# Kernel optimization log

Hardware: AMD Instinct MI355X
Metric: run time of the kernel (lower is better)

The kernel has to match this reference:

```python
import jax, jax.numpy as jnp
import numpy as np

B, ROWS, COLS, D, H = 64, 7, 7, 1280, 256
S, NEG, GRU_ROWS = 5, 16, 6  # pred_steps, neg_samples, rows processed by GRU


def setup_inputs() -> dict:
    key = jax.random.key(0)
    ks = jax.random.split(key, 10)
    sc = 0.05  # keep gates/tanh out of saturation
    return {
        "encodings": jax.random.normal(ks[0], (B, ROWS, COLS, D), jnp.float32),
        "hidden": jnp.zeros((1, 1, H), jnp.float32),
        "gru_w_ih": jax.random.normal(ks[1], (3 * H, D), jnp.float32) * sc,
        "gru_w_hh": jax.random.normal(ks[2], (3 * H, H), jnp.float32) * sc,
        "gru_b_ih": jax.random.normal(ks[3], (3 * H,), jnp.float32) * sc,
        "gru_b_hh": jax.random.normal(ks[4], (3 * H,), jnp.float32) * sc,
        "wk_w": jax.random.normal(ks[5], (S, D, H), jnp.float32) * sc,
        "wk_b": jax.random.normal(ks[6], (S, D), jnp.float32) * sc,
        "neg_rows": jax.random.randint(ks[7], (B, S, GRU_ROWS, COLS, NEG), 0, ROWS, jnp.int32),
        "neg_cols": jax.random.randint(ks[8], (B, S, GRU_ROWS, COLS, NEG), 0, COLS, jnp.int32),
    }


def _gru_contexts(encodings, hidden, w_ih, w_hh, b_ih, b_hh):
    # One GRU run per (image, column) over the first 6 rows, all batched together.
    x_seq = jnp.transpose(encodings[:, :GRU_ROWS], (1, 0, 2, 3)).reshape(GRU_ROWS, B * COLS, D)
    h0 = jnp.broadcast_to(hidden.reshape(1, H), (B * COLS, H))

    def step(h, x):
        gi = x @ w_ih.T + b_ih          # [N, 3H]
        gh = h @ w_hh.T + b_hh
        i_r, i_z, i_n = jnp.split(gi, 3, axis=-1)
        h_r, h_z, h_n = jnp.split(gh, 3, axis=-1)
        r = jax.nn.sigmoid(i_r + h_r)
        z = jax.nn.sigmoid(i_z + h_z)
        n = jnp.tanh(i_n + r * h_n)
        h_new = (1.0 - z) * n + z * h
        return h_new, h_new

    _, cs = jax.lax.scan(step, h0, x_seq)              # [6, B*7, H]
    return jnp.transpose(cs.reshape(GRU_ROWS, B, COLS, H), (1, 0, 2, 3))  # [B,6,7,H]


def reference(encodings, hidden, gru_w_ih, gru_w_hh, gru_b_ih, gru_b_hh,
              wk_w, wk_b, neg_rows, neg_cols):
    contexts = _gru_contexts(encodings, hidden, gru_w_ih, gru_w_hh, gru_b_ih, gru_b_hh)

    # Predictions for every step/row/col: hardtanh(Wk[s] c + b)   [B,S,6,7,D]
    preds = jnp.clip(jnp.einsum("brch,sdh->bsrcd", contexts, wk_w)
                     + wk_b[None, :, None, None, :], -1.0, 1.0)

    # Dot of every prediction with every patch encoding of the same image.
    enc_flat = encodings.reshape(B, ROWS * COLS, D)
    dots_all = jnp.einsum("bsrcd,bqd->bsrcq", preds, enc_flat)  # [B,S,6,7,49]

    # Positive: target is encodings[img, row, col] (as in the source).
    qpos = (jnp.arange(GRU_ROWS)[:, None] * COLS + jnp.arange(COLS)[None, :])  # [6,7]
    pos = jnp.take_along_axis(dots_all, qpos[None, None, :, :, None], axis=-1)  # [B,S,6,7,1]

    # Negatives: random (row,col) patches of the same image.
    neg_q = neg_rows * COLS + neg_cols                            # [B,S,6,7,NEG]
    neg = jnp.take_along_axis(dots_all, neg_q, axis=-1)

    dots = jnp.concatenate([pos, neg], axis=-1)                   # [B,S,6,7,1+NEG]
    loss_each = -jax.nn.log_softmax(dots, axis=-1)[..., 0]
    correct = (jnp.argmax(dots, axis=-1) == 0).astype(jnp.float32)

    # Valid predictions: row in range(6 - step)
    mask = ((jnp.arange(S)[:, None] + jnp.arange(GRU_ROWS)[None, :]) < GRU_ROWS)
    mask = mask.astype(jnp.float32)[None, :, :, None]             # [1,S,6,1]
    num_preds = jnp.sum(mask) * B * COLS

    loss = jnp.sum(loss_each * mask) / num_preds
    acc = jnp.sum(correct * mask) / num_preds
    return loss, acc
```

## Files before the change

kernel.cpp:

```cpp
#include <hip/hip_runtime.h>
#include <math.h>


typedef __bf16 bf16x8 __attribute__((ext_vector_type(8)));
typedef float  f32x4  __attribute__((ext_vector_type(4)));
typedef unsigned short u16;
typedef unsigned int u32;

__device__ inline u16 f2bf(float f) {
  unsigned int u = __float_as_uint(f);
  u += 0x7fff + ((u >> 16) & 1);
  return (u16)(u >> 16);
}

__device__ inline float bf2f(u16 b) {
  u32 u = (u32)b << 16;
  return __builtin_bit_cast(float, u);
}

__device__ inline void f2bf8(const float* s, u16* o) {
  float4 v0 = *(const float4*)s, v1 = *(const float4*)(s + 4);
  o[0] = f2bf(v0.x); o[1] = f2bf(v0.y); o[2] = f2bf(v0.z); o[3] = f2bf(v0.w);
  o[4] = f2bf(v1.x); o[5] = f2bf(v1.y); o[6] = f2bf(v1.z); o[7] = f2bf(v1.w);
}

__device__ inline bf16x8 lds_frag(const char* sm, int off) {
  return __builtin_bit_cast(bf16x8, *(const uint4*)(sm + off));
}

__device__ inline void gld_lds16(const void* g, void* l) {
  __builtin_amdgcn_global_load_lds(
      (const __attribute__((address_space(1))) u32*)g,
      (__attribute__((address_space(3))) u32*)l, 16, 0, 0);
}

__device__ inline float fast_sigmoid(float x) {
  float t = __builtin_amdgcn_exp2f(-1.44269504f * x);
  return __builtin_amdgcn_rcpf(1.f + t);
}
__device__ inline float fast_tanh(float x) {
  float xc = fminf(fmaxf(x, -9.f), 9.f);
  float t = __builtin_amdgcn_exp2f(2.88539008f * xc);
  return (t - 1.f) * __builtin_amdgcn_rcpf(t + 1.f);
}
__device__ inline float fast_exp(float x) {
  return __builtin_amdgcn_exp2f(1.44269504f * x);
}
__device__ inline float fast_log(float x) {
  return __builtin_amdgcn_logf(x) * 0.69314718f;
}

#define MFMA16(a, b, c) __builtin_amdgcn_mfma_f32_16x16x32_bf16(a, b, c, 0, 0, 0)

__global__ __launch_bounds__(256) void pack_all(
    const float* __restrict__ w_hh, const float* __restrict__ wk_w,
    const float* __restrict__ enc,  const float* __restrict__ w_ih,
    u16* __restrict__ whhpk, u16* __restrict__ wkwpk, u16* __restrict__ epk,
    u16* __restrict__ enc2,  u16* __restrict__ wih2, float* __restrict__ out)
{
  int tid = blockIdx.x * 256 + threadIdx.x;
  int lane = tid & 63;
  if (tid == 0) { out[0] = 0.f; out[1] = 0.f; }
  u16 o[8];
  if (tid < 655360) {
    int f = tid >> 6;
    int ks2 = f & 1, t1 = f >> 1;
    int w = t1 & 3, t2 = t1 >> 2;
    int ch = t2 % 20, b = t2 / 20;
    int q = w * 16 + (lane & 15);
    int d = ch * 64 + ks2 * 32 + (lane >> 4) * 8;
    if (q < 49) {
      f2bf8(&enc[(size_t)(b * 49 + q) * 1280 + d], o);
    } else {
#pragma unroll
      for (int j = 0; j < 8; ++j) o[j] = 0;
    }
    *(uint4*)&epk[(size_t)f * 512 + lane * 8] = *(uint4*)o;
    if (q < 42) {
      int r = q / 7, c = q - r * 7;
      int m = r * 448 + b * 7 + c;
      int by = m >> 7, row = m & 127;
      int k0 = d >> 6, slot = (d & 63) >> 3;
      int sl = slot ^ (row & 7);
      *(uint4*)&enc2[(size_t)((by * 20 + k0) * 1024 + row * 8 + sl) * 8] = *(uint4*)o;
    }
  } else if (tid < 679936) {
    int u = tid - 655360;
    int rest = u >> 6;
    int cb = rest >> 3, ks = rest & 7;
    int w = cb / 6, nf = cb % 6;
    int g = nf >> 1, half = nf & 1;
    int col = g * 256 + w * 32 + half * 16 + (lane & 15);
    int k = ks * 32 + (lane >> 4) * 8;
    f2bf8(&w_hh[(size_t)col * 256 + k], o);
    *(uint4*)&whhpk[(size_t)u * 8] = *(uint4*)o;
  } else if (tid < 884736) {
    int u = tid - 679936;
    int f = u >> 6;
    int ks = f & 7, t1 = f >> 3;
    int w = t1 & 3, t2 = t1 >> 2;
    int ch = t2 % 20, s = t2 / 20;
    f2bf8(&wk_w[((size_t)s * 1280 + ch * 64 + w * 16 + (lane & 15)) * 256
                + ks * 32 + (lane >> 4) * 8], o);
    *(uint4*)&wkwpk[(size_t)f * 512 + lane * 8] = *(uint4*)o;
  } else if (tid < 1007616) {
    int u = tid - 884736;
    int unit = u & 1023;
    int row = unit >> 3, sl = unit & 7;
    int tk = u >> 10;
    int k0 = tk % 20, bx = tk / 20;
    int slot = sl ^ (row & 7);
    f2bf8(&w_ih[(size_t)(bx * 128 + row) * 1280 + k0 * 64 + slot * 8], o);
    *(uint4*)&wih2[(size_t)u * 8] = *(uint4*)o;
  }
}

__global__ __launch_bounds__(256) void gi_mfma(
    const u16* __restrict__ enc2, const u16* __restrict__ wih2,
    const float* __restrict__ b_ih, u16* __restrict__ gib)
{
  const int bx = blockIdx.x, by = blockIdx.y;
  const int t = threadIdx.x, lane = t & 63, w = t >> 6;
  const int wr = w >> 1, wc = w & 1;

  __shared__ char sm[65536];
  const int wu = t & ~63;

  f32x4 acc[4][4];
#pragma unroll
  for (int i = 0; i < 4; ++i)
#pragma unroll
    for (int j = 0; j < 4; ++j) acc[i][j] = (f32x4){0.f, 0.f, 0.f, 0.f};

  const char* ga0 = (const char*)enc2 + ((size_t)(by * 20) << 14);
  const char* gb0 = (const char*)wih2 + ((size_t)(bx * 20) << 14);

#pragma unroll
  for (int j = 0; j < 4; ++j) {
    gld_lds16(ga0 + (j * 256 + t) * 16, sm + (j * 256 + wu) * 16);
    gld_lds16(gb0 + (j * 256 + t) * 16, sm + 16384 + (j * 256 + wu) * 16);
  }

  for (int k0c = 0; k0c < 20; ++k0c) {
    char* cur = sm + (k0c & 1) * 32768;
    if (k0c + 1 < 20) {
      char* nxt = sm + ((k0c + 1) & 1) * 32768;
      const char* ga = ga0 + ((size_t)(k0c + 1) << 14);
      const char* gb = gb0 + ((size_t)(k0c + 1) << 14);
#pragma unroll
      for (int j = 0; j < 4; ++j) {
        gld_lds16(ga + (j * 256 + t) * 16, nxt + (j * 256 + wu) * 16);
        gld_lds16(gb + (j * 256 + t) * 16, nxt + 16384 + (j * 256 + wu) * 16);
      }
      asm volatile("s_waitcnt vmcnt(8)" ::: "memory");
    } else {
      asm volatile("s_waitcnt vmcnt(0)" ::: "memory");
    }
    __builtin_amdgcn_s_barrier();

#pragma unroll
    for (int ks = 0; ks < 2; ++ks) {
      bf16x8 a[4], b[4];
#pragma unroll
      for (int i = 0; i < 4; ++i) {
        int arow = wr * 64 + i * 16 + (lane & 15);
        int akb  = (ks * 64 + (lane >> 4) * 16) ^ ((arow & 7) << 4);
        a[i] = lds_frag(cur, arow * 128 + akb);
        int brow = wc * 64 + i * 16 + (lane & 15);
        int bkb  = (ks * 64 + (lane >> 4) * 16) ^ ((brow & 7) << 4);
        b[i] = lds_frag(cur + 16384, brow * 128 + bkb);
      }
#pragma unroll
      for (int i = 0; i < 4; ++i)
#pragma unroll
        for (int jn = 0; jn < 4; ++jn)
          acc[i][jn] = MFMA16(a[i], b[jn], acc[i][jn]);
    }
    __builtin_amdgcn_s_barrier();
  }

#pragma unroll
  for (int i = 0; i < 4; ++i)
#pragma unroll
    for (int jn = 0; jn < 4; ++jn) {
      int gcol = bx * 128 + wc * 64 + jn * 16 + (lane & 15);
      float bias = b_ih[gcol];
#pragma unroll
      for (int r4 = 0; r4 < 4; ++r4) {
        int grow = by * 128 + wr * 64 + i * 16 + (lane >> 4) * 4 + r4;
        gib[(size_t)grow * 768 + gcol] = f2bf(acc[i][jn][r4] + bias);
      }
    }
}

__global__ __launch_bounds__(512) void gru_fused(
    const u16* __restrict__ whh_pk, const float* __restrict__ b_hh,
    const float* __restrict__ hidden, const u16* __restrict__ gib,
    u16* __restrict__ ctxb)
{
  const int n0 = blockIdx.x * 16;
  const int t = threadIdx.x, lane = t & 63, w = t >> 6;

  __shared__ char sm[16384 + 2 * 24576];
  const int GI0 = 16384;

  const int l15 = lane & 15;
  const int seq0 = (lane >> 4) * 4;
  const int hc0 = w * 32 + l15, hc1 = w * 32 + 16 + l15;

  const float br0 = b_hh[hc0],       br1 = b_hh[hc1];
  const float bz0 = b_hh[256 + hc0], bz1 = b_hh[256 + hc1];
  const float bn0 = b_hh[512 + hc0], bn1 = b_hh[512 + hc1];

#pragma unroll
  for (int i = 0; i < 3; ++i) {
    int chunk = w * 3 + i;
    gld_lds16(gib + (size_t)n0 * 768 + chunk * 512 + lane * 8,
              sm + GI0 + chunk * 1024);
  }

  float hold[2][4];
  {
    float h0 = hidden[hc0], h1 = hidden[hc1];
#pragma unroll
    for (int r4 = 0; r4 < 4; ++r4) { hold[0][r4] = h0; hold[1][r4] = h1; }
    u16 hb0 = f2bf(h0), hb1 = f2bf(h1);
#pragma unroll
    for (int r4 = 0; r4 < 4; ++r4) {
      int seq = seq0 + r4;
      *(u16*)(sm + seq * 512 + ((hc0 * 2) ^ ((seq & 7) << 4))) = hb0;
      *(u16*)(sm + seq * 512 + ((hc1 * 2) ^ ((seq & 7) << 4))) = hb1;
    }
  }

  bf16x8 bP[3][6];
  {
    const char* pkb0 = (const char*)whh_pk + w * 49152 + lane * 16;
#pragma unroll
    for (int j = 0; j < 3; ++j)
#pragma unroll
      for (int nf = 0; nf < 6; ++nf)
        bP[j][nf] = *(const bf16x8*)(pkb0 + nf * 8192 + j * 1024);
  }
  __syncthreads();

  for (int r = 0; r < 6; ++r) {
    const char* hb  = sm + (r & 1) * 8192;
    char* hbn       = sm + ((r + 1) & 1) * 8192;
    const char* gbr = sm + GI0 + (r & 1) * 24576;

    uintptr_t pa = (uintptr_t)whh_pk;
    asm volatile("" : "+v"(pa));
    const char* pkb = (const char*)pa + w * 49152 + lane * 16;

    f32x4 acc[6];
#pragma unroll
    for (int nf = 0; nf < 6; ++nf) acc[nf] = (f32x4){0.f, 0.f, 0.f, 0.f};

#pragma unroll
    for (int ks = 0; ks < 8; ++ks) {
      const int slot = ks % 3;
      bf16x8 a = lds_frag(hb, l15 * 512 +
                          ((ks * 64 + (lane >> 4) * 16) ^ ((l15 & 7) << 4)));
#pragma unroll
      for (int nf = 0; nf < 6; ++nf) acc[nf] = MFMA16(a, bP[slot][nf], acc[nf]);
      {
        const int nk = (ks + 3) & 7;
#pragma unroll
        for (int nf = 0; nf < 6; ++nf)
          bP[slot][nf] = *(const bf16x8*)(pkb + nf * 8192 + nk * 1024);
      }
    }

    if (r + 1 < 6) {
#pragma unroll
      for (int i = 0; i < 3; ++i) {
        int chunk = w * 3 + i;
        gld_lds16(gib + (size_t)((r + 1) * 448 + n0) * 768 + chunk * 512 + lane * 8,
                  sm + GI0 + ((r + 1) & 1) * 24576 + chunk * 1024);
      }
    }

#pragma unroll
    for (int r4 = 0; r4 < 4; ++r4) {
      int seq = seq0 + r4;
      float ir0 = bf2f(*(const u16*)(gbr + (size_t)(seq * 768 + hc0) * 2));
      float iz0 = bf2f(*(const u16*)(gbr + (size_t)(seq * 768 + 256 + hc0) * 2));
      float in0 = bf2f(*(const u16*)(gbr + (size_t)(seq * 768 + 512 + hc0) * 2));
      float ir1 = bf2f(*(const u16*)(gbr + (size_t)(seq * 768 + hc1) * 2));
      float iz1 = bf2f(*(const u16*)(gbr + (size_t)(seq * 768 + 256 + hc1) * 2));
      float in1 = bf2f(*(const u16*)(gbr + (size_t)(seq * 768 + 512 + hc1) * 2));
      {
        float rg = fast_sigmoid(ir0 + acc[0][r4] + br0);
        float zg = fast_sigmoid(iz0 + acc[2][r4] + bz0);
        float ng = fast_tanh(in0 + rg * (acc[4][r4] + bn0));
        float hnew = (1.f - zg) * ng + zg * hold[0][r4];
        hold[0][r4] = hnew;
        u16 hb16 = f2bf(hnew);
        *(u16*)(hbn + seq * 512 + ((hc0 * 2) ^ ((seq & 7) << 4))) = hb16;
        ctxb[(size_t)(r * 448 + n0 + seq) * 256 + hc0] = hb16;
      }
      {
        float rg = fast_sigmoid(ir1 + acc[1][r4] + br1);
        float zg = fast_sigmoid(iz1 + acc[3][r4] + bz1);
        float ng = fast_tanh(in1 + rg * (acc[5][r4] + bn1));
        float hnew = (1.f - zg) * ng + zg * hold[1][r4];
        hold[1][r4] = hnew;
        u16 hb16 = f2bf(hnew);
        *(u16*)(hbn + seq * 512 + ((hc1 * 2) ^ ((seq & 7) << 4))) = hb16;
        ctxb[(size_t)(r * 448 + n0 + seq) * 256 + hc1] = hb16;
      }
    }
    __syncthreads();
  }
}

template<int MF>
__device__ __forceinline__ void pd_body(
    int b, int s, int Ms, int t, int lane, int w, char* sm,
    const u16* __restrict__ ctxb, const u16* __restrict__ wkwpk,
    const float* __restrict__ wk_b, const u16* __restrict__ epk,
    const int* __restrict__ neg_rows, const int* __restrict__ neg_cols,
    float* __restrict__ out)
{
  const int PT_OFF = 24576;

#pragma unroll
  for (int j = 0; j < 6; ++j) {
    int u = j * 256 + t;
    int row = u >> 5, slot = u & 31;
    int rr = row < Ms ? row : 0;
    int r = rr / 7, c = rr - r * 7;
    uint4 v = *(const uint4*)&ctxb[((size_t)(r * 448 + b * 7 + c)) * 256 + slot * 8];
    int off = row * 512 + ((slot * 16) ^ ((row & 7) << 4));
    *(uint4*)(sm + off) = v;
  }
  __syncthreads();

  bf16x8 a1[MF][8];
#pragma unroll
  for (int m = 0; m < MF; ++m)
#pragma unroll
    for (int ks = 0; ks < 8; ++ks) {
      int row = m * 16 + (lane & 15);
      int kb  = (ks * 64 + (lane >> 4) * 16) ^ ((row & 7) << 4);
      a1[m][ks] = lds_frag(sm, row * 512 + kb);
    }

  f32x4 acc2[MF];
#pragma unroll
  for (int m = 0; m < MF; ++m) acc2[m] = (f32x4){0.f, 0.f, 0.f, 0.f};

  const char* wfB = (const char*)wkwpk + ((size_t)(s * 20) * 4 + w) * 8192 + lane * 16;
  const char* efB = (const char*)epk   + ((size_t)(b * 20) * 4 + w) * 2048 + lane * 16;
  const int colL = w * 16 + (lane & 15);

  bf16x8 wF[8];
#pragma unroll
  for (int ks = 0; ks < 8; ++ks)
    wF[ks] = *(const bf16x8*)(wfB + ks * 1024);

  for (int ch = 0; ch < 20; ++ch) {
    char* pt = sm + PT_OFF + (ch & 1) * 6144;

    f32x4 acc1[MF];
#pragma unroll
    for (int m = 0; m < MF; ++m) acc1[m] = (f32x4){0.f, 0.f, 0.f, 0.f};
#pragma unroll
    for (int ks = 0; ks < 8; ++ks) {
#pragma unroll
      for (int m = 0; m < MF; ++m) acc1[m] = MFMA16(a1[m][ks], wF[ks], acc1[m]);
    }
    if (ch + 1 < 20) {
      const char* wfn = wfB + (size_t)(ch + 1) * 4 * 8192;
#pragma unroll
      for (int ks = 0; ks < 8; ++ks)
        wF[ks] = *(const bf16x8*)(wfn + ks * 1024);
    }
    {
      float bias = wk_b[s * 1280 + ch * 64 + colL];
#pragma unroll
      for (int m = 0; m < MF; ++m)
#pragma unroll
        for (int r4 = 0; r4 < 4; ++r4) {
          float p = acc1[m][r4] + bias;
          p = fminf(fmaxf(p, -1.f), 1.f);
          int prow = m * 16 + (lane >> 4) * 4 + r4;
          *(u16*)(pt + prow * 128 + ((colL * 2) ^ ((prow & 7) << 4))) = f2bf(p);
        }
    }
    const char* ef = efB + (size_t)ch * 4 * 2048;
    bf16x8 e0 = *(const bf16x8*)ef;
    bf16x8 e1 = *(const bf16x8*)(ef + 1024);
    __syncthreads();

#pragma unroll
    for (int m = 0; m < MF; ++m) {
      int prow = m * 16 + (lane & 15);
      bf16x8 pf0 = lds_frag(pt, prow * 128 +
                            (((lane >> 4) * 16) ^ ((prow & 7) << 4)));
      acc2[m] = MFMA16(pf0, e0, acc2[m]);
      bf16x8 pf1 = lds_frag(pt, prow * 128 +
                            ((64 + (lane >> 4) * 16) ^ ((prow & 7) << 4)));
      acc2[m] = MFMA16(pf1, e1, acc2[m]);
    }
  }

  float* dtile = (float*)sm;
#pragma unroll
  for (int m = 0; m < MF; ++m)
#pragma unroll
    for (int r4 = 0; r4 < 4; ++r4) {
      int row = m * 16 + (lane >> 4) * 4 + r4;
      int q = w * 16 + (lane & 15);
      dtile[row * 65 + q] = acc2[m][r4];
    }
  __syncthreads();

  if (w == 0) {
    float lsum = 0.f, csum = 0.f;
    if (lane < Ms) {
      int rr = lane;
      int r = rr / 7, c = rr - r * 7;
      const float* drow = &dtile[rr * 65];
      float d0 = drow[rr];
      const int nbase = (((b * 5 + s) * 6 + r) * 7 + c) * 16;
      float mx = d0;
      float d[16];
#pragma unroll
      for (int j = 0; j < 16; ++j) {
        int q = neg_rows[nbase + j] * 7 + neg_cols[nbase + j];
        d[j] = drow[q];
        mx = fmaxf(mx, d[j]);
      }
      float se = fast_exp(d0 - mx);
#pragma unroll
      for (int j = 0; j < 16; ++j) se += fast_exp(d[j] - mx);
      lsum = -(d0 - mx - fast_log(se));
      csum = (d0 >= mx) ? 1.f : 0.f;
    }
#pragma unroll
    for (int off = 32; off > 0; off >>= 1) {
      lsum += __shfl_down(lsum, off);
      csum += __shfl_down(csum, off);
    }
    if (lane == 0) {
      atomicAdd(&out[0], lsum * (1.f / 8960.f));
      atomicAdd(&out[1], csum * (1.f / 8960.f));
    }
  }
}

__global__ __launch_bounds__(256) void fused_pd(
    const u16* __restrict__ ctxb, const u16* __restrict__ wkwpk,
    const float* __restrict__ wk_b, const u16* __restrict__ epk,
    const int* __restrict__ neg_rows, const int* __restrict__ neg_cols,
    float* __restrict__ out)
{
  const int b = blockIdx.x;
  const int s = blockIdx.y;
  const int Ms = (6 - s) * 7;
  const int t = threadIdx.x;
  const int lane = t & 63, w = t >> 6;

  __shared__ uint4 smem4[36864 / 16];
  char* sm = (char*)smem4;

  if (s < 2)      pd_body<3>(b, s, Ms, t, lane, w, sm, ctxb, wkwpk, wk_b, epk,
                             neg_rows, neg_cols, out);
  else if (s < 4) pd_body<2>(b, s, Ms, t, lane, w, sm, ctxb, wkwpk, wk_b, epk,
                             neg_rows, neg_cols, out);
  else            pd_body<1>(b, s, Ms, t, lane, w, sm, ctxb, wkwpk, wk_b, epk,
                             neg_rows, neg_cols, out);
}

extern "C" void kernel_launch(void* const* d_in, const int* in_sizes, int n_in,
                              void* d_out, int out_size, void* d_ws, size_t ws_size,
                              hipStream_t stream)
{
  const float* enc    = (const float*)d_in[0];
  const float* hidden = (const float*)d_in[1];
  const float* w_ih   = (const float*)d_in[2];
  const float* w_hh   = (const float*)d_in[3];
  const float* b_ih   = (const float*)d_in[4];
  const float* b_hh   = (const float*)d_in[5];
  const float* wk_w   = (const float*)d_in[6];
  const float* wk_b   = (const float*)d_in[7];
  const int* neg_rows = (const int*)d_in[8];
  const int* neg_cols = (const int*)d_in[9];
  float* out = (float*)d_out;

  u16*   gib   = (u16*)d_ws;
  u16*   ctxb  = gib + 6 * 448 * 768;
  u16*   whhpk = ctxb + 6 * 448 * 256;
  u16*   wkwpk = whhpk + 24576 * 8;
  u16*   epk   = wkwpk + 204800 * 8;
  u16*   enc2  = epk + 655360 * 8;
  u16*   wih2  = enc2 + 430080 * 8;

  pack_all<<<3936, 256, 0, stream>>>(w_hh, wk_w, enc, w_ih,
                                     whhpk, wkwpk, epk, enc2, wih2, out);

  gi_mfma<<<dim3(6, 21), 256, 0, stream>>>(enc2, wih2, b_ih, gib);

  gru_fused<<<28, 512, 0, stream>>>(whhpk, b_hh, hidden, gib, ctxb);

  fused_pd<<<dim3(64, 5), 256, 0, stream>>>(ctxb, wkwpk, wk_b, epk,
                                            neg_rows, neg_cols, out);
}
```

Before: 92.12 us.

## Merge all four stages into one cooperative persistent kernel with grid syncs

Replaces the four separate launches (pack, input-gate GEMM, GRU, prediction/dot) with a single cooperative kernel of 256 blocks of 512 threads, using grid.sync between stages. Each stage is adapted to the new block shape: gi uses 512 threads with smaller per-wave tiles, pd_body idles the upper four waves, and blocks 192+ run a second pd pass to cover step 4. The aim is to remove launch gaps and inter-kernel drain. In exchange it adds grid-wide barriers, leaves half the threads idle in the pd stage, and serialises step 4 work on some blocks.

```diff
diff --git a/kernel.cpp b/kernel.cpp
--- a/kernel.cpp
+++ b/kernel.cpp
@@ -1,5 +1,8 @@
 #include <hip/hip_runtime.h>
+#include <hip/hip_cooperative_groups.h>
 #include <math.h>
+
+namespace cg = cooperative_groups;
 
 
 typedef __bf16 bf16x8 __attribute__((ext_vector_type(8)));
@@ -52,15 +55,13 @@
 
 #define MFMA16(a, b, c) __builtin_amdgcn_mfma_f32_16x16x32_bf16(a, b, c, 0, 0, 0)
 
-__global__ __launch_bounds__(256) void pack_all(
-    const float* __restrict__ w_hh, const float* __restrict__ wk_w,
-    const float* __restrict__ enc,  const float* __restrict__ w_ih,
+__device__ __forceinline__ void pack_unit(
+    int tid, const float* __restrict__ w_hh, const float* __restrict__ wk_w,
+    const float* __restrict__ enc, const float* __restrict__ w_ih,
     u16* __restrict__ whhpk, u16* __restrict__ wkwpk, u16* __restrict__ epk,
-    u16* __restrict__ enc2,  u16* __restrict__ wih2, float* __restrict__ out)
-{
-  int tid = blockIdx.x * 256 + threadIdx.x;
+    u16* __restrict__ enc2,  u16* __restrict__ wih2)
+{
   int lane = tid & 63;
-  if (tid == 0) { out[0] = 0.f; out[1] = 0.f; }
   u16 o[8];
   if (tid < 655360) {
     int f = tid >> 6;
@@ -115,20 +116,19 @@
   }
 }
 
-__global__ __launch_bounds__(256) void gi_mfma(
+__device__ __forceinline__ void gi_body(
+    char* sm, int bid, int t,
     const u16* __restrict__ enc2, const u16* __restrict__ wih2,
     const float* __restrict__ b_ih, u16* __restrict__ gib)
 {
-  const int bx = blockIdx.x, by = blockIdx.y;
-  const int t = threadIdx.x, lane = t & 63, w = t >> 6;
+  const int bx = bid % 6, by = bid / 6;
+  const int lane = t & 63, w = t >> 6;
   const int wr = w >> 1, wc = w & 1;
-
-  __shared__ char sm[65536];
   const int wu = t & ~63;
 
-  f32x4 acc[4][4];
-#pragma unroll
-  for (int i = 0; i < 4; ++i)
+  f32x4 acc[2][4];
+#pragma unroll
+  for (int i = 0; i < 2; ++i)
 #pragma unroll
     for (int j = 0; j < 4; ++j) acc[i][j] = (f32x4){0.f, 0.f, 0.f, 0.f};
 
@@ -136,9 +136,9 @@
   const char* gb0 = (const char*)wih2 + ((size_t)(bx * 20) << 14);
 
 #pragma unroll
-  for (int j = 0; j < 4; ++j) {
-    gld_lds16(ga0 + (j * 256 + t) * 16, sm + (j * 256 + wu) * 16);
-    gld_lds16(gb0 + (j * 256 + t) * 16, sm + 16384 + (j * 256 + wu) * 16);
+  for (int j = 0; j < 2; ++j) {
+    gld_lds16(ga0 + (j * 512 + t) * 16, sm + (j * 512 + wu) * 16);
+    gld_lds16(gb0 + (j * 512 + t) * 16, sm + 16384 + (j * 512 + wu) * 16);
   }
 
   for (int k0c = 0; k0c < 20; ++k0c) {
@@ -148,11 +148,11 @@
       const char* ga = ga0 + ((size_t)(k0c + 1) << 14);
       const char* gb = gb0 + ((size_t)(k0c + 1) << 14);
 #pragma unroll
-      for (int j = 0; j < 4; ++j) {
-        gld_lds16(ga + (j * 256 + t) * 16, nxt + (j * 256 + wu) * 16);
-        gld_lds16(gb + (j * 256 + t) * 16, nxt + 16384 + (j * 256 + wu) * 16);
-      }
-      asm volatile("s_waitcnt vmcnt(8)" ::: "memory");
+      for (int j = 0; j < 2; ++j) {
+        gld_lds16(ga + (j * 512 + t) * 16, nxt + (j * 512 + wu) * 16);
+        gld_lds16(gb + (j * 512 + t) * 16, nxt + 16384 + (j * 512 + wu) * 16);
+      }
+      asm volatile("s_waitcnt vmcnt(4)" ::: "memory");
     } else {
       asm volatile("s_waitcnt vmcnt(0)" ::: "memory");
     }
@@ -160,18 +160,21 @@
 
 #pragma unroll
     for (int ks = 0; ks < 2; ++ks) {
-      bf16x8 a[4], b[4];
-#pragma unroll
-      for (int i = 0; i < 4; ++i) {
-        int arow = wr * 64 + i * 16 + (lane & 15);
+      bf16x8 a[2], b[4];
+#pragma unroll
+      for (int i = 0; i < 2; ++i) {
+        int arow = wr * 32 + i * 16 + (lane & 15);
         int akb  = (ks * 64 + (lane >> 4) * 16) ^ ((arow & 7) << 4);
         a[i] = lds_frag(cur, arow * 128 + akb);
-        int brow = wc * 64 + i * 16 + (lane & 15);
+      }
+#pragma unroll
+      for (int jn = 0; jn < 4; ++jn) {
+        int brow = wc * 64 + jn * 16 + (lane & 15);
         int bkb  = (ks * 64 + (lane >> 4) * 16) ^ ((brow & 7) << 4);
-        b[i] = lds_frag(cur + 16384, brow * 128 + bkb);
-      }
-#pragma unroll
-      for (int i = 0; i < 4; ++i)
+        b[jn] = lds_frag(cur + 16384, brow * 128 + bkb);
+      }
+#pragma unroll
+      for (int i = 0; i < 2; ++i)
 #pragma unroll
         for (int jn = 0; jn < 4; ++jn)
           acc[i][jn] = MFMA16(a[i], b[jn], acc[i][jn]);
@@ -180,28 +183,27 @@
   }
 
 #pragma unroll
-  for (int i = 0; i < 4; ++i)
+  for (int i = 0; i < 2; ++i)
 #pragma unroll
     for (int jn = 0; jn < 4; ++jn) {
       int gcol = bx * 128 + wc * 64 + jn * 16 + (lane & 15);
       float bias = b_ih[gcol];
 #pragma unroll
       for (int r4 = 0; r4 < 4; ++r4) {
-        int grow = by * 128 + wr * 64 + i * 16 + (lane >> 4) * 4 + r4;
+        int grow = by * 128 + wr * 32 + i * 16 + (lane >> 4) * 4 + r4;
         gib[(size_t)grow * 768 + gcol] = f2bf(acc[i][jn][r4] + bias);
       }
     }
 }
 
-__global__ __launch_bounds__(512) void gru_fused(
+__device__ __forceinline__ void gru_body(
+    char* sm, int bid, int t,
     const u16* __restrict__ whh_pk, const float* __restrict__ b_hh,
     const float* __restrict__ hidden, const u16* __restrict__ gib,
     u16* __restrict__ ctxb)
 {
-  const int n0 = blockIdx.x * 16;
-  const int t = threadIdx.x, lane = t & 63, w = t >> 6;
-
-  __shared__ char sm[16384 + 2 * 24576];
+  const int n0 = bid * 16;
+  const int lane = t & 63, w = t >> 6;
   const int GI0 = 16384;
 
   const int l15 = lane & 15;
@@ -324,10 +326,11 @@
     float* __restrict__ out)
 {
   const int PT_OFF = 24576;
-
-#pragma unroll
-  for (int j = 0; j < 6; ++j) {
-    int u = j * 256 + t;
+  const bool act = (w < 4);
+
+#pragma unroll
+  for (int j = 0; j < 3; ++j) {
+    int u = j * 512 + t;
     int row = u >> 5, slot = u & 31;
     int rr = row < Ms ? row : 0;
     int r = rr / 7, c = rr - r * 7;
@@ -338,46 +341,51 @@
   __syncthreads();
 
   bf16x8 a1[MF][8];
-#pragma unroll
-  for (int m = 0; m < MF; ++m)
-#pragma unroll
-    for (int ks = 0; ks < 8; ++ks) {
-      int row = m * 16 + (lane & 15);
-      int kb  = (ks * 64 + (lane >> 4) * 16) ^ ((row & 7) << 4);
-      a1[m][ks] = lds_frag(sm, row * 512 + kb);
-    }
+  if (act) {
+#pragma unroll
+    for (int m = 0; m < MF; ++m)
+#pragma unroll
+      for (int ks = 0; ks < 8; ++ks) {
+        int row = m * 16 + (lane & 15);
+        int kb  = (ks * 64 + (lane >> 4) * 16) ^ ((row & 7) << 4);
+        a1[m][ks] = lds_frag(sm, row * 512 + kb);
+      }
+  }
 
   f32x4 acc2[MF];
 #pragma unroll
   for (int m = 0; m < MF; ++m) acc2[m] = (f32x4){0.f, 0.f, 0.f, 0.f};
 
-  const char* wfB = (const char*)wkwpk + ((size_t)(s * 20) * 4 + w) * 8192 + lane * 16;
-  const char* efB = (const char*)epk   + ((size_t)(b * 20) * 4 + w) * 2048 + lane * 16;
-  const int colL = w * 16 + (lane & 15);
+  const char* wfB = (const char*)wkwpk + ((size_t)(s * 20) * 4 + (w & 3)) * 8192 + lane * 16;
+  const char* efB = (const char*)epk   + ((size_t)(b * 20) * 4 + (w & 3)) * 2048 + lane * 16;
+  const int colL = (w & 3) * 16 + (lane & 15);
 
   bf16x8 wF[8];
-#pragma unroll
-  for (int ks = 0; ks < 8; ++ks)
-    wF[ks] = *(const bf16x8*)(wfB + ks * 1024);
+  if (act) {
+#pragma unroll
+    for (int ks = 0; ks < 8; ++ks)
+      wF[ks] = *(const bf16x8*)(wfB + ks * 1024);
+  }
 
   for (int ch = 0; ch < 20; ++ch) {
     char* pt = sm + PT_OFF + (ch & 1) * 6144;
-
-    f32x4 acc1[MF];
-#pragma unroll
-    for (int m = 0; m < MF; ++m) acc1[m] = (f32x4){0.f, 0.f, 0.f, 0.f};
-#pragma unroll
-    for (int ks = 0; ks < 8; ++ks) {
-#pragma unroll
-      for (int m = 0; m < MF; ++m) acc1[m] = MFMA16(a1[m][ks], wF[ks], acc1[m]);
-    }
-    if (ch + 1 < 20) {
-      const char* wfn = wfB + (size_t)(ch + 1) * 4 * 8192;
-#pragma unroll
-      for (int ks = 0; ks < 8; ++ks)
-        wF[ks] = *(const bf16x8*)(wfn + ks * 1024);
-    }
-    {
+    bf16x8 e0{}, e1{};
+
+    if (act) {
+      f32x4 acc1[MF];
+#pragma unroll
+      for (int m = 0; m < MF; ++m) acc1[m] = (f32x4){0.f, 0.f, 0.f, 0.f};
+#pragma unroll
+      for (int ks = 0; ks < 8; ++ks) {
+#pragma unroll
+        for (int m = 0; m < MF; ++m) acc1[m] = MFMA16(a1[m][ks], wF[ks], acc1[m]);
+      }
+      if (ch + 1 < 20) {
+        const char* wfn = wfB + (size_t)(ch + 1) * 4 * 8192;
+#pragma unroll
+        for (int ks = 0; ks < 8; ++ks)
+          wF[ks] = *(const bf16x8*)(wfn + ks * 1024);
+      }
       float bias = wk_b[s * 1280 + ch * 64 + colL];
 #pragma unroll
       for (int m = 0; m < MF; ++m)
@@ -388,33 +396,37 @@
           int prow = m * 16 + (lane >> 4) * 4 + r4;
           *(u16*)(pt + prow * 128 + ((colL * 2) ^ ((prow & 7) << 4))) = f2bf(p);
         }
-    }
-    const char* ef = efB + (size_t)ch * 4 * 2048;
-    bf16x8 e0 = *(const bf16x8*)ef;
-    bf16x8 e1 = *(const bf16x8*)(ef + 1024);
+      const char* ef = efB + (size_t)ch * 4 * 2048;
+      e0 = *(const bf16x8*)ef;
+      e1 = *(const bf16x8*)(ef + 1024);
+    }
     __syncthreads();
 
-#pragma unroll
-    for (int m = 0; m < MF; ++m) {
-      int prow = m * 16 + (lane & 15);
-      bf16x8 pf0 = lds_frag(pt, prow * 128 +
-                            (((lane >> 4) * 16) ^ ((prow & 7) << 4)));
-      acc2[m] = MFMA16(pf0, e0, acc2[m]);
-      bf16x8 pf1 = lds_frag(pt, prow * 128 +
-                            ((64 + (lane >> 4) * 16) ^ ((prow & 7) << 4)));
-      acc2[m] = MFMA16(pf1, e1, acc2[m]);
+    if (act) {
+#pragma unroll
+      for (int m = 0; m < MF; ++m) {
+        int prow = m * 16 + (lane & 15);
+        bf16x8 pf0 = lds_frag(pt, prow * 128 +
+                              (((lane >> 4) * 16) ^ ((prow & 7) << 4)));
+        acc2[m] = MFMA16(pf0, e0, acc2[m]);
+        bf16x8 pf1 = lds_frag(pt, prow * 128 +
+                              ((64 + (lane >> 4) * 16) ^ ((prow & 7) << 4)));
+        acc2[m] = MFMA16(pf1, e1, acc2[m]);
+      }
     }
   }
 
   float* dtile = (float*)sm;
-#pragma unroll
-  for (int m = 0; m < MF; ++m)
-#pragma unroll
-    for (int r4 = 0; r4 < 4; ++r4) {
-      int row = m * 16 + (lane >> 4) * 4 + r4;
-      int q = w * 16 + (lane & 15);
-      dtile[row * 65 + q] = acc2[m][r4];
-    }
+  if (act) {
+#pragma unroll
+    for (int m = 0; m < MF; ++m)
+#pragma unroll
+      for (int r4 = 0; r4 < 4; ++r4) {
+        int row = m * 16 + (lane >> 4) * 4 + r4;
+        int q = (w & 3) * 16 + (lane & 15);
+        dtile[row * 65 + q] = acc2[m][r4];
+      }
+  }
   __syncthreads();
 
   if (w == 0) {
@@ -449,29 +461,65 @@
       atomicAdd(&out[1], csum * (1.f / 8960.f));
     }
   }
-}
-
-__global__ __launch_bounds__(256) void fused_pd(
+  __syncthreads();
+}
+
+__device__ __forceinline__ void pd_run(
+    int b, int s, char* sm, int t,
     const u16* __restrict__ ctxb, const u16* __restrict__ wkwpk,
     const float* __restrict__ wk_b, const u16* __restrict__ epk,
     const int* __restrict__ neg_rows, const int* __restrict__ neg_cols,
     float* __restrict__ out)
 {
-  const int b = blockIdx.x;
-  const int s = blockIdx.y;
   const int Ms = (6 - s) * 7;
-  const int t = threadIdx.x;
   const int lane = t & 63, w = t >> 6;
-
-  __shared__ uint4 smem4[36864 / 16];
-  char* sm = (char*)smem4;
-
   if (s < 2)      pd_body<3>(b, s, Ms, t, lane, w, sm, ctxb, wkwpk, wk_b, epk,
                              neg_rows, neg_cols, out);
   else if (s < 4) pd_body<2>(b, s, Ms, t, lane, w, sm, ctxb, wkwpk, wk_b, epk,
                              neg_rows, neg_cols, out);
   else            pd_body<1>(b, s, Ms, t, lane, w, sm, ctxb, wkwpk, wk_b, epk,
                              neg_rows, neg_cols, out);
+}
+
+__global__ void __launch_bounds__(512) mega(
+    const float* __restrict__ w_hh, const float* __restrict__ wk_w,
+    const float* __restrict__ enc,  const float* __restrict__ w_ih,
+    const float* __restrict__ b_ih, const float* __restrict__ b_hh,
+    const float* __restrict__ hidden, const float* __restrict__ wk_b,
+    const int* __restrict__ neg_rows, const int* __restrict__ neg_cols,
+    u16* __restrict__ whhpk, u16* __restrict__ wkwpk, u16* __restrict__ epk,
+    u16* __restrict__ enc2,  u16* __restrict__ wih2,
+    u16* __restrict__ gib,   u16* __restrict__ ctxb, float* __restrict__ out)
+{
+  extern __shared__ char sm[];
+  cg::grid_group grid = cg::this_grid();
+  const int bid = blockIdx.x;
+  const int t = threadIdx.x;
+
+  if (bid == 0 && t == 0) { out[0] = 0.f; out[1] = 0.f; }
+#pragma unroll
+  for (int it = 0; it < 8; ++it) {
+    int tid = it * 131072 + bid * 512 + t;
+    if (tid < 1007616)
+      pack_unit(tid, w_hh, wk_w, enc, w_ih, whhpk, wkwpk, epk, enc2, wih2);
+  }
+  grid.sync();
+
+  if (bid < 126)
+    gi_body(sm, bid, t, enc2, wih2, b_ih, gib);
+  grid.sync();
+
+  if (bid < 28)
+    gru_body(sm, bid, t, whhpk, b_hh, hidden, gib, ctxb);
+  grid.sync();
+
+  {
+    int s = bid >> 6;
+    int b = bid & 63;
+    pd_run(b, s, sm, t, ctxb, wkwpk, wk_b, epk, neg_rows, neg_cols, out);
+    if (bid >= 192)
+      pd_run(bid - 192, 4, sm, t, ctxb, wkwpk, wk_b, epk, neg_rows, neg_cols, out);
+  }
 }
 
 extern "C" void kernel_launch(void* const* d_in, const int* in_sizes, int n_in,
@@ -498,13 +546,13 @@
   u16*   enc2  = epk + 655360 * 8;
   u16*   wih2  = enc2 + 430080 * 8;
 
-  pack_all<<<3936, 256, 0, stream>>>(w_hh, wk_w, enc, w_ih,
-                                     whhpk, wkwpk, epk, enc2, wih2, out);
-
-  gi_mfma<<<dim3(6, 21), 256, 0, stream>>>(enc2, wih2, b_ih, gib);
-
-  gru_fused<<<28, 512, 0, stream>>>(whhpk, b_hh, hidden, gib, ctxb);
-
-  fused_pd<<<dim3(64, 5), 256, 0, stream>>>(ctxb, wkwpk, wk_b, epk,
-                                            neg_rows, neg_cols, out);
-}
+  void* args[] = {
+    (void*)&w_hh, (void*)&wk_w, (void*)&enc, (void*)&w_ih,
+    (void*)&b_ih, (void*)&b_hh, (void*)&hidden, (void*)&wk_b,
+    (void*)&neg_rows, (void*)&neg_cols,
+    (void*)&whhpk, (void*)&wkwpk, (void*)&epk, (void*)&enc2, (void*)&wih2,
+    (void*)&gib, (void*)&ctxb, (void*)&out
+  };
+  hipLaunchCooperativeKernel((const void*)mega, dim3(256), dim3(512),
+                             args, 65536, stream);
+}
```

After: 199.1 us. 2.16x slower.

## Split packing so non-GEMM packs overlap the input-gate GEMM kernel

Applied to the files above, without the earlier changes.

The single pack kernel is split in two. The first converts only the inputs the gi GEMM needs (encodings to enc2, w_ih to wih2). The remaining packs (epk, whhpk, wkwpk) now run as extra blocks appended to the gi GEMM launch, so that conversion overlaps the 126 GEMM blocks instead of running before them. The enc2 packing is rewritten to iterate over the output layout, which costs one extra read of the encodings relative to the shared path. The shared-memory declaration now applies to the pack blocks too, which may limit their occupancy.

```diff
diff --git a/kernel.cpp b/kernel.cpp
--- a/kernel.cpp
+++ b/kernel.cpp
@@ -52,59 +52,27 @@
 
 #define MFMA16(a, b, c) __builtin_amdgcn_mfma_f32_16x16x32_bf16(a, b, c, 0, 0, 0)
 
-__global__ __launch_bounds__(256) void pack_all(
-    const float* __restrict__ w_hh, const float* __restrict__ wk_w,
-    const float* __restrict__ enc,  const float* __restrict__ w_ih,
-    u16* __restrict__ whhpk, u16* __restrict__ wkwpk, u16* __restrict__ epk,
-    u16* __restrict__ enc2,  u16* __restrict__ wih2, float* __restrict__ out)
+__global__ __launch_bounds__(256) void packA(
+    const float* __restrict__ enc, const float* __restrict__ w_ih,
+    u16* __restrict__ enc2, u16* __restrict__ wih2, float* __restrict__ out)
 {
   int tid = blockIdx.x * 256 + threadIdx.x;
-  int lane = tid & 63;
   if (tid == 0) { out[0] = 0.f; out[1] = 0.f; }
   u16 o[8];
-  if (tid < 655360) {
-    int f = tid >> 6;
-    int ks2 = f & 1, t1 = f >> 1;
-    int w = t1 & 3, t2 = t1 >> 2;
-    int ch = t2 % 20, b = t2 / 20;
-    int q = w * 16 + (lane & 15);
-    int d = ch * 64 + ks2 * 32 + (lane >> 4) * 8;
-    if (q < 49) {
-      f2bf8(&enc[(size_t)(b * 49 + q) * 1280 + d], o);
-    } else {
-#pragma unroll
-      for (int j = 0; j < 8; ++j) o[j] = 0;
-    }
-    *(uint4*)&epk[(size_t)f * 512 + lane * 8] = *(uint4*)o;
-    if (q < 42) {
-      int r = q / 7, c = q - r * 7;
-      int m = r * 448 + b * 7 + c;
-      int by = m >> 7, row = m & 127;
-      int k0 = d >> 6, slot = (d & 63) >> 3;
-      int sl = slot ^ (row & 7);
-      *(uint4*)&enc2[(size_t)((by * 20 + k0) * 1024 + row * 8 + sl) * 8] = *(uint4*)o;
-    }
-  } else if (tid < 679936) {
-    int u = tid - 655360;
-    int rest = u >> 6;
-    int cb = rest >> 3, ks = rest & 7;
-    int w = cb / 6, nf = cb % 6;
-    int g = nf >> 1, half = nf & 1;
-    int col = g * 256 + w * 32 + half * 16 + (lane & 15);
-    int k = ks * 32 + (lane >> 4) * 8;
-    f2bf8(&w_hh[(size_t)col * 256 + k], o);
-    *(uint4*)&whhpk[(size_t)u * 8] = *(uint4*)o;
-  } else if (tid < 884736) {
-    int u = tid - 679936;
-    int f = u >> 6;
-    int ks = f & 7, t1 = f >> 3;
-    int w = t1 & 3, t2 = t1 >> 2;
-    int ch = t2 % 20, s = t2 / 20;
-    f2bf8(&wk_w[((size_t)s * 1280 + ch * 64 + w * 16 + (lane & 15)) * 256
-                + ks * 32 + (lane >> 4) * 8], o);
-    *(uint4*)&wkwpk[(size_t)f * 512 + lane * 8] = *(uint4*)o;
-  } else if (tid < 1007616) {
-    int u = tid - 884736;
+  if (tid < 430080) {
+    int u = tid;
+    int unit = u & 1023;
+    int row = unit >> 3, sl = unit & 7;
+    int tk = u >> 10;
+    int k0 = tk % 20, by = tk / 20;
+    int m = by * 128 + row;
+    int r = m / 448, n = m - r * 448;
+    int b = n / 7, c = n - b * 7;
+    int slot = sl ^ (row & 7);
+    f2bf8(&enc[(size_t)(b * 49 + r * 7 + c) * 1280 + k0 * 64 + slot * 8], o);
+    *(uint4*)&enc2[(size_t)u * 8] = *(uint4*)o;
+  } else if (tid < 552960) {
+    int u = tid - 430080;
     int unit = u & 1023;
     int row = unit >> 3, sl = unit & 7;
     int tk = u >> 10;
@@ -115,15 +83,61 @@
   }
 }
 
-__global__ __launch_bounds__(256) void gi_mfma(
+__global__ __launch_bounds__(256) void gi_packB(
     const u16* __restrict__ enc2, const u16* __restrict__ wih2,
-    const float* __restrict__ b_ih, u16* __restrict__ gib)
+    const float* __restrict__ b_ih, u16* __restrict__ gib,
+    const float* __restrict__ w_hh, const float* __restrict__ wk_w,
+    const float* __restrict__ enc,
+    u16* __restrict__ whhpk, u16* __restrict__ wkwpk, u16* __restrict__ epk)
 {
-  const int bx = blockIdx.x, by = blockIdx.y;
-  const int t = threadIdx.x, lane = t & 63, w = t >> 6;
+  __shared__ char sm[65536];
+  const int bid = blockIdx.x;
+  const int t = threadIdx.x;
+
+  if (bid >= 126) {
+    int tid = (bid - 126) * 256 + t;
+    int lane = tid & 63;
+    u16 o[8];
+    if (tid < 655360) {
+      int f = tid >> 6;
+      int ks2 = f & 1, t1 = f >> 1;
+      int w = t1 & 3, t2 = t1 >> 2;
+      int ch = t2 % 20, b = t2 / 20;
+      int q = w * 16 + (lane & 15);
+      int d = ch * 64 + ks2 * 32 + (lane >> 4) * 8;
+      if (q < 49) {
+        f2bf8(&enc[(size_t)(b * 49 + q) * 1280 + d], o);
+      } else {
+#pragma unroll
+        for (int j = 0; j < 8; ++j) o[j] = 0;
+      }
+      *(uint4*)&epk[(size_t)f * 512 + lane * 8] = *(uint4*)o;
+    } else if (tid < 679936) {
+      int u = tid - 655360;
+      int rest = u >> 6;
+      int cb = rest >> 3, ks = rest & 7;
+      int w = cb / 6, nf = cb % 6;
+      int g = nf >> 1, half = nf & 1;
+      int col = g * 256 + w * 32 + half * 16 + (lane & 15);
+      int k = ks * 32 + (lane >> 4) * 8;
+      f2bf8(&w_hh[(size_t)col * 256 + k], o);
+      *(uint4*)&whhpk[(size_t)u * 8] = *(uint4*)o;
+    } else if (tid < 884736) {
+      int u = tid - 679936;
+      int f = u >> 6;
+      int ks = f & 7, t1 = f >> 3;
+      int w = t1 & 3, t2 = t1 >> 2;
+      int ch = t2 % 20, s = t2 / 20;
+      f2bf8(&wk_w[((size_t)s * 1280 + ch * 64 + w * 16 + (lane & 15)) * 256
+                  + ks * 32 + (lane >> 4) * 8], o);
+      *(uint4*)&wkwpk[(size_t)f * 512 + lane * 8] = *(uint4*)o;
+    }
+    return;
+  }
+
+  const int bx = bid % 6, by = bid / 6;
+  const int lane = t & 63, w = t >> 6;
   const int wr = w >> 1, wc = w & 1;
-
-  __shared__ char sm[65536];
   const int wu = t & ~63;
 
   f32x4 acc[4][4];
@@ -498,10 +512,10 @@
   u16*   enc2  = epk + 655360 * 8;
   u16*   wih2  = enc2 + 430080 * 8;
 
-  pack_all<<<3936, 256, 0, stream>>>(w_hh, wk_w, enc, w_ih,
-                                     whhpk, wkwpk, epk, enc2, wih2, out);
-
-  gi_mfma<<<dim3(6, 21), 256, 0, stream>>>(enc2, wih2, b_ih, gib);
+  packA<<<2160, 256, 0, stream>>>(enc, w_ih, enc2, wih2, out);
+
+  gi_packB<<<3582, 256, 0, stream>>>(enc2, wih2, b_ih, gib,
+                                     w_hh, wk_w, enc, whhpk, wkwpk, epk);
 
   gru_fused<<<28, 512, 0, stream>>>(whhpk, b_hh, hidden, gib, ctxb);
 
```

After: 87.07 us, median of 3. 5.5% less time.
